# Performance work log

Measured on AMD Instinct MI355X. Metric: run time of the kernel, lower is better.

The kernel has to match this reference:

```python
import jax, jax.numpy as jnp
import numpy as np

DIM = 512
QK = 16
PDIM = DIM // 2
B, H, W = 8, 64, 64
EPS = 1e-5


def setup_inputs() -> dict:
    key = jax.random.key(0)
    ks = jax.random.split(key, 8)
    x = jax.random.normal(ks[0], (B, DIM, H, W), dtype=jnp.float32)
    # GroupNorm(1 group) affine params over pdim channels
    gn_w = jax.random.normal(ks[1], (PDIM,), dtype=jnp.float32) * 0.02 + 1.0
    gn_b = jax.random.normal(ks[2], (PDIM,), dtype=jnp.float32) * 0.02
    # qkv: 1x1 conv pdim -> 2*qk + pdim, BN folded into weight+bias
    w_qkv = jax.random.normal(ks[3], (2 * QK + PDIM, PDIM), dtype=jnp.float32) * (PDIM ** -0.5)
    b_qkv = jax.random.normal(ks[4], (2 * QK + PDIM,), dtype=jnp.float32) * 0.02
    # proj: SiLU then 1x1 conv dim -> dim, BN folded into weight+bias
    w_proj = jax.random.normal(ks[5], (DIM, DIM), dtype=jnp.float32) * (DIM ** -0.5)
    b_proj = jax.random.normal(ks[6], (DIM,), dtype=jnp.float32) * 0.02
    return {"x": x, "gn_w": gn_w, "gn_b": gn_b, "w_qkv": w_qkv,
            "b_qkv": b_qkv, "w_proj": w_proj, "b_proj": b_proj}


def reference(x, gn_w, gn_b, w_qkv, b_qkv, w_proj, b_proj):
    b, c, h, w = x.shape
    scale = QK ** -0.5
    x1, x2 = x[:, :PDIM], x[:, PDIM:]
    # GroupNorm with 1 group: normalize over (C, H, W) per sample
    mu = jnp.mean(x1, axis=(1, 2, 3), keepdims=True)
    var = jnp.var(x1, axis=(1, 2, 3), keepdims=True)
    x1n = (x1 - mu) * jax.lax.rsqrt(var + EPS)
    x1n = x1n * gn_w[None, :, None, None] + gn_b[None, :, None, None]
    # 1x1 conv (BN folded) as channel GEMM; flatten spatial -> N = H*W
    x1f = x1n.reshape(b, PDIM, h * w)                       # [B, pdim, N]
    qkv = jnp.einsum('oc,bcn->bon', w_qkv, x1f) + b_qkv[None, :, None]
    q, k, v = qkv[:, :QK], qkv[:, QK:2 * QK], qkv[:, 2 * QK:]
    # attn[b, n, m] = sum_c q[b,c,n] k[b,c,m] * scale
    attn = jnp.einsum('bcn,bcm->bnm', q, k) * scale          # [B, N, N]
    attn = jax.nn.softmax(attn, axis=-1)
    # x1 = v @ attn^T : out[b,c,n] = sum_m v[b,c,m] attn[b,n,m]
    x1o = jnp.einsum('bcm,bnm->bcn', v, attn).reshape(b, PDIM, h, w)
    y = jnp.concatenate([x1o, x2], axis=1)                   # [B, dim, H, W]
    y = jax.nn.silu(y)
    yf = y.reshape(b, DIM, h * w)
    out = jnp.einsum('oc,bcn->bon', w_proj, yf) + b_proj[None, :, None]
    return out.reshape(b, DIM, h, w)
```

## Files before the change

kernel.cpp:

```cpp
#include <hip/hip_runtime.h>
#include <math.h>

typedef unsigned short u16;
typedef unsigned int u32;
typedef __attribute__((ext_vector_type(4))) u16 u16x4;
typedef __attribute__((ext_vector_type(8))) short bf16x8;
typedef __attribute__((ext_vector_type(4))) float f32x4;

#define MFMA16(a, b, c) __builtin_amdgcn_mfma_f32_16x16x32_bf16(a, b, c, 0, 0, 0)

namespace {
constexpr int BATCH = 8;
constexpr int CDIM  = 512;
constexpr int PD    = 256;
constexpr int NPIX  = 4096;
constexpr int NTOT  = PD * NPIX;
constexpr float LOG2E = 1.44269504088896f;

constexpr int OFF_PART = 0;
constexpr int OFF_STAT = 2048;

constexpr size_t U16_BASE = 139264;
constexpr size_t QT_ELEMS = (size_t)BATCH * NPIX * 16;
constexpr size_t V_ELEMS  = (size_t)BATCH * PD * NPIX;
constexpr size_t Y_ELEMS  = (size_t)BATCH * NPIX * CDIM;
constexpr size_t WP_ELEMS = (size_t)CDIM * CDIM;
constexpr size_t WQ_ELEMS = 288 * 256;
}

__device__ __forceinline__ u16 f2bf(float f) {
    union { float f; u32 u; } v; v.f = f;
    return (u16)((v.u + 0x7fffu + ((v.u >> 16) & 1u)) >> 16);
}
__device__ __forceinline__ u32 cvtpk(float lo, float hi) {
    u32 r;
    asm("v_cvt_pk_bf16_f32 %0, %1, %2" : "=v"(r) : "v"(lo), "v"(hi));
    return r;
}

__global__ __launch_bounds__(256) void k_stats_partial(const float* __restrict__ x,
                                                       float* __restrict__ ws) {
    int b = blockIdx.y, chunk = blockIdx.x, t = threadIdx.x;
    const float4* x4 = reinterpret_cast<const float4*>(
        x + (size_t)b * CDIM * NPIX + (size_t)chunk * 16384);
    float s = 0.f, sq = 0.f;
#pragma unroll
    for (int i = 0; i < 16; ++i) {
        float4 v = x4[i * 256 + t];
        s  += v.x + v.y + v.z + v.w;
        sq += v.x * v.x + v.y * v.y + v.z * v.z + v.w * v.w;
    }
    for (int off = 32; off; off >>= 1) {
        s  += __shfl_down(s, off);
        sq += __shfl_down(sq, off);
    }
    __shared__ float red[8];
    int wid = t >> 6, lane = t & 63;
    if (lane == 0) { red[wid * 2] = s; red[wid * 2 + 1] = sq; }
    __syncthreads();
    if (t == 0) {
        float S = red[0] + red[2] + red[4] + red[6];
        float Q = red[1] + red[3] + red[5] + red[7];
        ws[OFF_PART + (b * 64 + chunk) * 2]     = S;
        ws[OFF_PART + (b * 64 + chunk) * 2 + 1] = Q;
    }
}

__global__ __launch_bounds__(64) void k_stats_final(float* __restrict__ ws) {
    int b = blockIdx.x, t = threadIdx.x;
    float s = ws[OFF_PART + (b * 64 + t) * 2];
    float q = ws[OFF_PART + (b * 64 + t) * 2 + 1];
    for (int off = 32; off; off >>= 1) {
        s += __shfl_down(s, off);
        q += __shfl_down(q, off);
    }
    if (t == 0) {
        float mean = s / (float)NTOT;
        float var  = q / (float)NTOT - mean * mean;
        ws[OFF_STAT + b * 2]     = mean;
        ws[OFF_STAT + b * 2 + 1] = rsqrtf(var + 1e-5f);
    }
}

__global__ __launch_bounds__(256) void k_cvt2(const float* __restrict__ wp,
                                              const float* __restrict__ wq,
                                              u16* __restrict__ wpb,
                                              u16* __restrict__ wqb) {
    int bx = blockIdx.x;
    const float* src = (bx < 256) ? wp : wq;
    u16* dst = (bx < 256) ? wpb : wqb;
    int base = (bx < 256) ? bx * 1024 : (bx - 256) * 1024;
    int i = base + threadIdx.x * 4;
    float4 v = *reinterpret_cast<const float4*>(src + i);
    u16x4 o;
    o.x = f2bf(v.x); o.y = f2bf(v.y); o.z = f2bf(v.z); o.w = f2bf(v.w);
    *reinterpret_cast<u16x4*>(dst + i) = o;
}

__global__ __launch_bounds__(256) void k_prep(const float* __restrict__ x,
        const float* __restrict__ gnw, const float* __restrict__ gnb,
        const float* __restrict__ wsf, u16* __restrict__ xn, u16* __restrict__ yb) {
    int b = blockIdx.z, yy = blockIdx.y, n0 = blockIdx.x * 64, t = threadIdx.x;
    __shared__ u16 T[64][72];
    int c = t >> 2, nb = (t & 3) * 16;
    if (yy < 4) {
        int ca = yy * 64 + c;
        float mu = wsf[OFF_STAT + b * 2], rs = wsf[OFF_STAT + b * 2 + 1];
        float a = rs * gnw[ca];
        float sh = gnb[ca] - mu * a;
        const float* xb = x + ((size_t)b * CDIM + ca) * NPIX;
#pragma unroll
        for (int j = 0; j < 4; ++j) {
            float4 v = *reinterpret_cast<const float4*>(xb + n0 + nb + j * 4);
            T[nb + j * 4 + 0][c] = f2bf(v.x * a + sh);
            T[nb + j * 4 + 1][c] = f2bf(v.y * a + sh);
            T[nb + j * 4 + 2][c] = f2bf(v.z * a + sh);
            T[nb + j * 4 + 3][c] = f2bf(v.w * a + sh);
        }
        __syncthreads();
        int n = t >> 2, cb = (t & 3) * 16;
        u16* dst = xn + ((size_t)b * NPIX + n0 + n) * PD + yy * 64 + cb;
#pragma unroll
        for (int j = 0; j < 4; ++j)
            *reinterpret_cast<u16x4*>(dst + j * 4) =
                *reinterpret_cast<u16x4*>(&T[n][cb + j * 4]);
    } else {
        int c0 = (yy - 4) * 64;
        const float* xb = x + ((size_t)b * CDIM + PD + c0 + c) * NPIX;
#pragma unroll
        for (int j = 0; j < 4; ++j) {
            float4 v = *reinterpret_cast<const float4*>(xb + n0 + nb + j * 4);
            T[nb + j * 4 + 0][c] = f2bf(v.x / (1.f + __expf(-v.x)));
            T[nb + j * 4 + 1][c] = f2bf(v.y / (1.f + __expf(-v.y)));
            T[nb + j * 4 + 2][c] = f2bf(v.z / (1.f + __expf(-v.z)));
            T[nb + j * 4 + 3][c] = f2bf(v.w / (1.f + __expf(-v.w)));
        }
        __syncthreads();
        int n = t >> 2, cb = (t & 3) * 16;
        u16* dst = yb + ((size_t)b * NPIX + n0 + n) * CDIM + PD + c0 + cb;
#pragma unroll
        for (int j = 0; j < 4; ++j)
            *reinterpret_cast<u16x4*>(dst + j * 4) =
                *reinterpret_cast<u16x4*>(&T[n][cb + j * 4]);
    }
}

__global__ __launch_bounds__(256) void k_qkv(const u16* __restrict__ xn,
        const u16* __restrict__ wq, const float* __restrict__ bqkv,
        u16* __restrict__ qt, u16* __restrict__ kt, u16* __restrict__ vb) {
    int b = blockIdx.z, o0 = blockIdx.y * 32, n0 = blockIdx.x * 256;
    int t = threadIdx.x, w = t >> 6, l = t & 63, lg = l >> 4, lr = l & 15;
    int nbase = n0 + w * 64;
    const u16* xnb = xn + (size_t)b * NPIX * PD;
    const f32x4 z4 = {0.f, 0.f, 0.f, 0.f};
    f32x4 acc[2][4];
#pragma unroll
    for (int i = 0; i < 2; ++i)
#pragma unroll
        for (int j = 0; j < 4; ++j) acc[i][j] = z4;

#pragma unroll
    for (int k0 = 0; k0 < PD; k0 += 32) {
        bf16x8 xf[4], wf[2];
#pragma unroll
        for (int nf = 0; nf < 4; ++nf)
            xf[nf] = *reinterpret_cast<const bf16x8*>(
                xnb + (size_t)(nbase + nf * 16 + lr) * PD + k0 + lg * 8);
#pragma unroll
        for (int of = 0; of < 2; ++of)
            wf[of] = *reinterpret_cast<const bf16x8*>(
                wq + (size_t)(o0 + of * 16 + lr) * PD + k0 + lg * 8);
#pragma unroll
        for (int of = 0; of < 2; ++of)
#pragma unroll
            for (int nf = 0; nf < 4; ++nf)
                acc[of][nf] = MFMA16(xf[nf], wf[of], acc[of][nf]);
    }

    if (o0 == 0) {
#pragma unroll
        for (int of = 0; of < 2; ++of) {
            int o = of * 16 + lr;
            float bias = bqkv[o];
            float sc = (of == 0) ? 0.25f * LOG2E : 1.0f;
            u16* dst = (of == 0) ? (qt + (size_t)b * NPIX * 16 + lr)
                                 : (kt + (size_t)b * NPIX * 16 + lr);
#pragma unroll
            for (int nf = 0; nf < 4; ++nf) {
#pragma unroll
                for (int r = 0; r < 4; ++r) {
                    int n = nbase + nf * 16 + 4 * lg + r;
                    dst[(size_t)n * 16] = f2bf((acc[of][nf][r] + bias) * sc);
                }
            }
        }
    } else {
        u16* vout = vb + (size_t)b * PD * NPIX;
#pragma unroll
        for (int of = 0; of < 2; ++of) {
            int c = o0 - 32 + of * 16 + lr;
            float bias = bqkv[32 + c];
#pragma unroll
            for (int nf = 0; nf < 4; ++nf) {
                u16x4 pw;
                pw.x = f2bf(acc[of][nf][0] + bias);
                pw.y = f2bf(acc[of][nf][1] + bias);
                pw.z = f2bf(acc[of][nf][2] + bias);
                pw.w = f2bf(acc[of][nf][3] + bias);
                int nblk = (nbase >> 3) + nf * 2 + (lg >> 1);
                *reinterpret_cast<u16x4*>(
                    vout + (size_t)nblk * 2048 + c * 8 + (lg & 1) * 4) = pw;
            }
        }
    }
}

__global__ __launch_bounds__(512) void k_attn_pv(const u16* __restrict__ qt,
        const u16* __restrict__ kt, const u16* __restrict__ vb,
        u16* __restrict__ yb) {
    int bid = blockIdx.x;
    int b = bid & 7, q0 = (bid >> 3) * 64;
    int t = threadIdx.x, w = t >> 6, l = t & 63, lg = l >> 4, lr = l & 15;
    int band = w & 3, mfb = w >> 2;
    __shared__ u16 Pl[16384];
    __shared__ float Ls[2][64];

    const u16* Qt = qt + ((size_t)b * NPIX + q0) * 16;

    const bf16x8 zf = {0, 0, 0, 0, 0, 0, 0, 0};
    bf16x8 qf = zf;
    if (lg < 2)
        qf = *reinterpret_cast<const bf16x8*>(Qt + (band * 16 + lr) * 16 + lg * 8);

    const u16* kp  = kt + (size_t)b * NPIX * 16 + (size_t)(mfb * 16 + lr) * 16 + lg * 8;
    const u16* vp0 = vb + (size_t)b * PD * NPIX + lg * 2048 + (size_t)(w * 32 + lr) * 8;
    const u16* vp1 = vp0 + 128;

    float lp = 0.f;
    const f32x4 z4 = {0.f, 0.f, 0.f, 0.f};
    f32x4 acc[2][4];
#pragma unroll
    for (int cf = 0; cf < 2; ++cf)
#pragma unroll
        for (int nf = 0; nf < 4; ++nf) acc[cf][nf] = z4;

    int n = band * 16 + lr;
    int swz = (n & 7) << 3;
    int wrb = (n * 64 + mfb * 16 + 4 * lg) ^ swz;

    int bufo = 0;
    for (int it = 0; it < 32; ++it) {
#pragma unroll
        for (int f = 0; f < 4; ++f) {
            int h = f >> 1, i = f & 1;
            bf16x8 kf = zf;
            if (lg < 2)
                kf = *reinterpret_cast<const bf16x8*>(kp + h * 1024 + i * 512);
            f32x4 s = MFMA16(kf, qf, z4);
            float p0 = exp2f(s[0]);
            float p1 = exp2f(s[1]);
            float p2 = exp2f(s[2]);
            float p3 = exp2f(s[3]);
            lp += (p0 + p1) + (p2 + p3);
            uint2 pw;
            pw.x = cvtpk(p0, p1);
            pw.y = cvtpk(p2, p3);
            *reinterpret_cast<uint2*>(
                &Pl[bufo + h * 4096 + (wrb ^ (i * 32))]) = pw;
        }
        __syncthreads();
#pragma unroll
        for (int sl = 0; sl < 4; ++sl) {
            int h = sl >> 1, ks = sl & 1;
            bf16x8 vf0 = *reinterpret_cast<const bf16x8*>(
                vp0 + (h * 8 + ks * 4) * 2048);
            bf16x8 vf1 = *reinterpret_cast<const bf16x8*>(
                vp1 + (h * 8 + ks * 4) * 2048);
#pragma unroll
            for (int nf = 0; nf < 4; ++nf) {
                int nn = nf * 16 + lr;
                bf16x8 pf = *reinterpret_cast<const bf16x8*>(
                    &Pl[bufo + h * 4096 +
                        ((nn * 64 + ks * 32 + lg * 8) ^ ((nn & 7) << 3))]);
                acc[0][nf] = MFMA16(vf0, pf, acc[0][nf]);
                acc[1][nf] = MFMA16(vf1, pf, acc[1][nf]);
            }
        }
        kp += 2048; vp0 += 32768; vp1 += 32768;
        bufo ^= 8192;
    }
    lp += __shfl_xor(lp, 16);
    lp += __shfl_xor(lp, 32);
    if (l < 16) Ls[mfb][band * 16 + l] = lp;
    __syncthreads();
    float invl[4];
#pragma unroll
    for (int nf = 0; nf < 4; ++nf)
        invl[nf] = 1.f / (Ls[0][nf * 16 + lr] + Ls[1][nf * 16 + lr]);
    u16* yrow = yb + (size_t)b * NPIX * CDIM;
#pragma unroll
    for (int nf = 0; nf < 4; ++nf) {
        int nq = q0 + nf * 16 + lr;
#pragma unroll
        for (int cf = 0; cf < 2; ++cf) {
            u16x4 pw;
#pragma unroll
            for (int r = 0; r < 4; ++r) {
                float v = acc[cf][nf][r] * invl[nf];
                pw[r] = f2bf(v / (1.f + __expf(-v)));
            }
            *reinterpret_cast<u16x4*>(
                yrow + (size_t)nq * CDIM + w * 32 + cf * 16 + 4 * lg) = pw;
        }
    }
}

__global__ __launch_bounds__(256) void k_proj_mfma(const u16* __restrict__ wb,
        const u16* __restrict__ yb, const float* __restrict__ bproj,
        float* __restrict__ out) {
    int b = blockIdx.z, n0 = blockIdx.x * 128, o0 = blockIdx.y * 128;
    int t = threadIdx.x, w = t >> 6, l = t & 63, lg = l >> 4, lr = l & 15;
    int wo = w & 1, wn = w >> 1;
    int obase = o0 + wo * 64, nbase = n0 + wn * 64;
    const u16* ybb = yb + (size_t)b * NPIX * CDIM;
    const f32x4 z4 = {0.f, 0.f, 0.f, 0.f};
    f32x4 acc[4][4];
#pragma unroll
    for (int i = 0; i < 4; ++i)
#pragma unroll
        for (int j = 0; j < 4; ++j) acc[i][j] = z4;

    for (int k0 = 0; k0 < CDIM; k0 += 32) {
        bf16x8 af[4], bfr[4];
#pragma unroll
        for (int of = 0; of < 4; ++of)
            af[of] = *reinterpret_cast<const bf16x8*>(
                wb + (size_t)(obase + of * 16 + lr) * CDIM + k0 + lg * 8);
#pragma unroll
        for (int nf = 0; nf < 4; ++nf)
            bfr[nf] = *reinterpret_cast<const bf16x8*>(
                ybb + (size_t)(nbase + nf * 16 + lr) * CDIM + k0 + lg * 8);
#pragma unroll
        for (int of = 0; of < 4; ++of)
#pragma unroll
            for (int nf = 0; nf < 4; ++nf)
                acc[of][nf] = MFMA16(af[of], bfr[nf], acc[of][nf]);
    }
#pragma unroll
    for (int of = 0; of < 4; ++of) {
        int o = obase + of * 16 + 4 * lg;
#pragma unroll
        for (int r = 0; r < 4; ++r) {
            float bb = bproj[o + r];
#pragma unroll
            for (int nf = 0; nf < 4; ++nf)
                out[((size_t)b * CDIM + o + r) * NPIX + nbase + nf * 16 + lr] =
                    acc[of][nf][r] + bb;
        }
    }
}

extern "C" void kernel_launch(void* const* d_in, const int* in_sizes, int n_in,
                              void* d_out, int out_size, void* d_ws, size_t ws_size,
                              hipStream_t stream) {
    const float* x     = (const float*)d_in[0];
    const float* gnw   = (const float*)d_in[1];
    const float* gnb   = (const float*)d_in[2];
    const float* wqkv  = (const float*)d_in[3];
    const float* bqkv  = (const float*)d_in[4];
    const float* wproj = (const float*)d_in[5];
    const float* bproj = (const float*)d_in[6];
    float* out = (float*)d_out;
    float* wsf = (float*)d_ws;

    u16* qtp = (u16*)d_ws + U16_BASE;
    u16* ktp = qtp + QT_ELEMS;
    u16* vbp = ktp + QT_ELEMS;
    u16* ybp = vbp + V_ELEMS;
    u16* wbp = ybp + Y_ELEMS;
    u16* wqb = wbp + WP_ELEMS;
    u16* xnp = wqb + WQ_ELEMS;

    k_stats_partial<<<dim3(64, 8), 256, 0, stream>>>(x, wsf);
    k_stats_final<<<8, 64, 0, stream>>>(wsf);
    k_cvt2<<<328, 256, 0, stream>>>(wproj, wqkv, wbp, wqb);
    k_prep<<<dim3(64, 8, 8), 256, 0, stream>>>(x, gnw, gnb, wsf, xnp, ybp);
    k_qkv<<<dim3(16, 9, 8), 256, 0, stream>>>(xnp, wqb, bqkv, qtp, ktp, vbp);
    k_attn_pv<<<512, 512, 0, stream>>>(qtp, ktp, vbp, ybp);
    k_proj_mfma<<<dim3(32, 4, 8), 256, 0, stream>>>(wbp, ybp, bproj, out);
}
```

Before: 228.1 us.

## Store bf16 operands in k-chunked [K/8][N][8] layout for coalesced MFMA loads

Measured after the change: 187.0 us. 18.0% less time.

```diff
diff --git a/kernel.cpp b/kernel.cpp
--- a/kernel.cpp
+++ b/kernel.cpp
@@ -26,6 +26,7 @@
 constexpr size_t Y_ELEMS  = (size_t)BATCH * NPIX * CDIM;
 constexpr size_t WP_ELEMS = (size_t)CDIM * CDIM;
 constexpr size_t WQ_ELEMS = 288 * 256;
+
 }
 
 __device__ __forceinline__ u16 f2bf(float f) {
@@ -86,15 +87,22 @@
                                               const float* __restrict__ wq,
                                               u16* __restrict__ wpb,
                                               u16* __restrict__ wqb) {
-    int bx = blockIdx.x;
-    const float* src = (bx < 256) ? wp : wq;
-    u16* dst = (bx < 256) ? wpb : wqb;
-    int base = (bx < 256) ? bx * 1024 : (bx - 256) * 1024;
-    int i = base + threadIdx.x * 4;
-    float4 v = *reinterpret_cast<const float4*>(src + i);
-    u16x4 o;
-    o.x = f2bf(v.x); o.y = f2bf(v.y); o.z = f2bf(v.z); o.w = f2bf(v.w);
-    *reinterpret_cast<u16x4*>(dst + i) = o;
+    int bx = blockIdx.x, t = threadIdx.x;
+    if (bx < 256) {
+        int i = bx * 1024 + t * 4;
+        int o = i >> 9, k = i & 511;
+        float4 v = *reinterpret_cast<const float4*>(wp + i);
+        u16x4 out;
+        out.x = f2bf(v.x); out.y = f2bf(v.y); out.z = f2bf(v.z); out.w = f2bf(v.w);
+        *reinterpret_cast<u16x4*>(wpb + (k >> 3) * 4096 + o * 8 + (k & 7)) = out;
+    } else {
+        int i = (bx - 256) * 1024 + t * 4;
+        int o = i >> 8, k = i & 255;
+        float4 v = *reinterpret_cast<const float4*>(wq + i);
+        u16x4 out;
+        out.x = f2bf(v.x); out.y = f2bf(v.y); out.z = f2bf(v.z); out.w = f2bf(v.w);
+        *reinterpret_cast<u16x4*>(wqb + (k >> 3) * 2304 + o * 8 + (k & 7)) = out;
+    }
 }
 
 __global__ __launch_bounds__(256) void k_prep(const float* __restrict__ x,
@@ -118,12 +126,14 @@
             T[nb + j * 4 + 3][c] = f2bf(v.w * a + sh);
         }
         __syncthreads();
-        int n = t >> 2, cb = (t & 3) * 16;
-        u16* dst = xn + ((size_t)b * NPIX + n0 + n) * PD + yy * 64 + cb;
-#pragma unroll
-        for (int j = 0; j < 4; ++j)
-            *reinterpret_cast<u16x4*>(dst + j * 4) =
-                *reinterpret_cast<u16x4*>(&T[n][cb + j * 4]);
+        int n = n0 + (t >> 2), cb = (t & 3) * 16;
+        u16* dstb = xn + (size_t)b * NPIX * PD;
+#pragma unroll
+        for (int j = 0; j < 4; ++j) {
+            int cg = yy * 64 + cb + j * 4;
+            *reinterpret_cast<u16x4*>(dstb + (size_t)(cg >> 3) * 32768 + n * 8 + (cg & 7)) =
+                *reinterpret_cast<u16x4*>(&T[t >> 2][cb + j * 4]);
+        }
     } else {
         int c0 = (yy - 4) * 64;
         const float* xb = x + ((size_t)b * CDIM + PD + c0 + c) * NPIX;
@@ -136,12 +146,14 @@
             T[nb + j * 4 + 3][c] = f2bf(v.w / (1.f + __expf(-v.w)));
         }
         __syncthreads();
-        int n = t >> 2, cb = (t & 3) * 16;
-        u16* dst = yb + ((size_t)b * NPIX + n0 + n) * CDIM + PD + c0 + cb;
-#pragma unroll
-        for (int j = 0; j < 4; ++j)
-            *reinterpret_cast<u16x4*>(dst + j * 4) =
-                *reinterpret_cast<u16x4*>(&T[n][cb + j * 4]);
+        int n = n0 + (t >> 2), cb = (t & 3) * 16;
+        u16* dstb = yb + (size_t)b * NPIX * CDIM;
+#pragma unroll
+        for (int j = 0; j < 4; ++j) {
+            int cg = PD + c0 + cb + j * 4;
+            *reinterpret_cast<u16x4*>(dstb + (size_t)(cg >> 3) * 32768 + n * 8 + (cg & 7)) =
+                *reinterpret_cast<u16x4*>(&T[t >> 2][cb + j * 4]);
+        }
     }
 }
 
@@ -165,11 +177,11 @@
 #pragma unroll
         for (int nf = 0; nf < 4; ++nf)
             xf[nf] = *reinterpret_cast<const bf16x8*>(
-                xnb + (size_t)(nbase + nf * 16 + lr) * PD + k0 + lg * 8);
+                xnb + (size_t)((k0 >> 3) + lg) * 32768 + (nbase + nf * 16 + lr) * 8);
 #pragma unroll
         for (int of = 0; of < 2; ++of)
             wf[of] = *reinterpret_cast<const bf16x8*>(
-                wq + (size_t)(o0 + of * 16 + lr) * PD + k0 + lg * 8);
+                wq + (size_t)((k0 >> 3) + lg) * 2304 + (o0 + of * 16 + lr) * 8);
 #pragma unroll
         for (int of = 0; of < 2; ++of)
 #pragma unroll
@@ -297,12 +309,13 @@
 #pragma unroll
     for (int nf = 0; nf < 4; ++nf)
         invl[nf] = 1.f / (Ls[0][nf * 16 + lr] + Ls[1][nf * 16 + lr]);
-    u16* yrow = yb + (size_t)b * NPIX * CDIM;
+    u16* ybase = yb + (size_t)b * NPIX * CDIM;
 #pragma unroll
     for (int nf = 0; nf < 4; ++nf) {
         int nq = q0 + nf * 16 + lr;
 #pragma unroll
         for (int cf = 0; cf < 2; ++cf) {
+            int cg = w * 32 + cf * 16 + 4 * lg;
             u16x4 pw;
 #pragma unroll
             for (int r = 0; r < 4; ++r) {
@@ -310,7 +323,7 @@
                 pw[r] = f2bf(v / (1.f + __expf(-v)));
             }
             *reinterpret_cast<u16x4*>(
-                yrow + (size_t)nq * CDIM + w * 32 + cf * 16 + 4 * lg) = pw;
+                ybase + (size_t)(cg >> 3) * 32768 + nq * 8 + (cg & 7)) = pw;
         }
     }
 }
@@ -335,11 +348,11 @@
 #pragma unroll
         for (int of = 0; of < 4; ++of)
             af[of] = *reinterpret_cast<const bf16x8*>(
-                wb + (size_t)(obase + of * 16 + lr) * CDIM + k0 + lg * 8);
+                wb + (size_t)((k0 >> 3) + lg) * 4096 + (obase + of * 16 + lr) * 8);
 #pragma unroll
         for (int nf = 0; nf < 4; ++nf)
             bfr[nf] = *reinterpret_cast<const bf16x8*>(
-                ybb + (size_t)(nbase + nf * 16 + lr) * CDIM + k0 + lg * 8);
+                ybb + (size_t)((k0 >> 3) + lg) * 32768 + (nbase + nf * 16 + lr) * 8);
 #pragma unroll
         for (int of = 0; of < 4; ++of)
 #pragma unroll
```
